# Kernel tuning notes

Measured on AMD Instinct MI355X. Metric: run time of the kernel, lower is better.

Reference implementation:

```python
import jax, jax.numpy as jnp
import numpy as np

ALPHA = 0.25          # VQLayer commitment weight
KL_WEIGHT = 0.01      # settings.kl_weight (repo global)
ENTROPY_WEIGHT = 0.1  # settings.entropy_weight (repo global)


def _forward(x, W0, b0, W1, b1, Wmu, bmu, Wvar, bvar, protos, eps):
    # MLP encoder: input_dim -> 64 -> output_dim, relu after each layer
    h = jax.nn.relu(x @ W0.T + b0)
    h = jax.nn.relu(h @ W1.T + b1)
    logvar = h @ Wvar.T + bvar
    mu = h @ Wmu.T + bmu
    # reparameterize
    latents = mu + eps * jnp.exp(0.5 * logvar)  # [B, D]

    # squared euclidean distances to prototypes: [B, P]
    dists = (jnp.sum(latents ** 2, axis=1, keepdims=True)
             + jnp.sum(protos ** 2, axis=1)
             - 2.0 * latents @ protos.T)
    idx = jnp.argmin(dists, axis=1)              # [B]
    quantized = protos[idx]                      # == one_hot @ protos

    commitment_loss = jnp.mean((jax.lax.stop_gradient(quantized) - latents) ** 2)
    embedding_loss = jnp.mean((quantized - jax.lax.stop_gradient(latents)) ** 2)
    vq_loss = commitment_loss * ALPHA + embedding_loss

    # categorical entropy of mean soft assignment
    logdist = jax.nn.log_softmax(-dists, axis=1)
    soft_dist = jnp.mean(jnp.exp(logdist), axis=0) + 1e-6
    soft_dist = soft_dist / jnp.sum(soft_dist)
    ent = jnp.sum(-soft_dist * jnp.log(soft_dist))
    vq_loss = vq_loss + ENTROPY_WEIGHT * ent

    # straight-through estimator
    quantized = latents + jax.lax.stop_gradient(quantized - latents)

    divergence = jnp.mean(-0.5 * jnp.sum(1.0 + logvar - mu ** 2 - jnp.exp(logvar), axis=1))
    total_loss = KL_WEIGHT * divergence + vq_loss
    return quantized, total_loss, divergence


def setup_inputs() -> dict:
    key = jax.random.key(0)
    ks = jax.random.split(key, 12)
    B, IN, HID, D, P = 32768, 1024, 64, 512, 2048

    def lin(k, fan_in, fan_out):
        bound = 1.0 / np.sqrt(fan_in)
        k1, k2 = jax.random.split(k)
        W = jax.random.uniform(k1, (fan_out, fan_in), jnp.float32, -bound, bound)
        b = jax.random.uniform(k2, (fan_out,), jnp.float32, -bound, bound)
        return W, b

    W0, b0 = lin(ks[0], IN, HID)
    W1, b1 = lin(ks[1], HID, D)
    Wmu, bmu = lin(ks[2], D, D)
    Wvar, bvar = lin(ks[3], D, D)
    protos = jax.random.uniform(ks[4], (P, D), jnp.float32, -1.0 / P, 1.0 / P)
    x = jax.random.normal(ks[5], (B, IN), jnp.float32)
    eps = jax.random.normal(ks[6], (B, D), jnp.float32)
    return {"x": x, "W0": W0, "b0": b0, "W1": W1, "b1": b1,
            "Wmu": Wmu, "bmu": bmu, "Wvar": Wvar, "bvar": bvar,
            "protos": protos, "eps": eps}


def reference(x, W0, b0, W1, b1, Wmu, bmu, Wvar, bvar, protos, eps):
    return _forward(x, W0, b0, W1, b1, Wmu, bmu, Wvar, bvar, protos, eps)
```

## Files before the change

kernel.cpp:

```cpp
#include <hip/hip_runtime.h>
#include <math.h>

#define B_N 32768
#define IN_DIM 1024
#define HID 64
#define D_DIM 512
#define P_N 2048

typedef __attribute__((ext_vector_type(8))) short s16x8;
typedef __attribute__((ext_vector_type(4))) float f32x4;

__device__ __forceinline__ unsigned short f2bf(float f) {
    unsigned u = __float_as_uint(f);
    return (unsigned short)((u + 0x7fffu + ((u >> 16) & 1u)) >> 16);
}
__device__ __forceinline__ float bf2f(unsigned short v) {
    return __uint_as_float(((unsigned)v) << 16);
}

__device__ __forceinline__ void gl_lds(const void* gsrc, void* ldst) {
    __builtin_amdgcn_global_load_lds(
        (const __attribute__((address_space(1))) unsigned int*)gsrc,
        (__attribute__((address_space(3))) unsigned int*)ldst, 16, 0, 0);
}

__device__ __forceinline__ s16x8 pack8(const float* s) {
    float4 x = *(const float4*)s;
    float4 y = *(const float4*)(s + 4);
    s16x8 o;
    o[0] = (short)f2bf(x.x); o[1] = (short)f2bf(x.y);
    o[2] = (short)f2bf(x.z); o[3] = (short)f2bf(x.w);
    o[4] = (short)f2bf(y.x); o[5] = (short)f2bf(y.y);
    o[6] = (short)f2bf(y.z); o[7] = (short)f2bf(y.w);
    return o;
}

__global__ __launch_bounds__(256) void k_prep(const float* __restrict__ protos,
                                              const float* __restrict__ Wmu,
                                              const float* __restrict__ Wvar,
                                              const float* __restrict__ W0,
                                              const float* __restrict__ W1,
                                              unsigned short* __restrict__ pb16,
                                              float* __restrict__ pnorm,
                                              unsigned short* __restrict__ wmv16,
                                              unsigned short* __restrict__ w0pack,
                                              unsigned short* __restrict__ w1pack) {
    int gid = blockIdx.x * 256 + threadIdx.x;
    if (gid < 131072) {
        int row = gid >> 6, k8 = gid & 63;
        const float* s = protos + (size_t)row * 512 + k8 * 8;
        float4 x = *(const float4*)s;
        float4 y = *(const float4*)(s + 4);
        s16x8 o;
        o[0] = (short)f2bf(x.x); o[1] = (short)f2bf(x.y);
        o[2] = (short)f2bf(x.z); o[3] = (short)f2bf(x.w);
        o[4] = (short)f2bf(y.x); o[5] = (short)f2bf(y.y);
        o[6] = (short)f2bf(y.z); o[7] = (short)f2bf(y.w);
        ((s16x8*)pb16)[(size_t)row * 64 + k8] = o;
        float ss = x.x * x.x + x.y * x.y + x.z * x.z + x.w * x.w +
                   y.x * y.x + y.y * y.y + y.z * y.z + y.w * y.w;
#pragma unroll
        for (int d = 1; d < 64; d <<= 1) ss += __shfl_xor(ss, d);
        if ((threadIdx.x & 63) == 0) pnorm[row] = ss;
    } else if (gid < 196608) {
        int a = gid - 131072;
        int row = a >> 6, k8 = a & 63;
        int g = row >> 5, i = row & 31;
        const float* s = (i < 16 ? Wmu + (size_t)(g * 16 + i) * 512
                                 : Wvar + (size_t)(g * 16 + i - 16) * 512) + k8 * 8;
        ((s16x8*)wmv16)[(size_t)row * 64 + k8] = pack8(s);
    } else if (gid < 204800) {
        int a = gid - 196608;
        int row = a >> 7, k8 = a & 127;
        int K32 = k8 >> 2;
        int lane = (row & 15) | ((k8 & 3) << 4);
        ((s16x8*)w0pack)[((size_t)(row >> 4) * 32 + K32) * 64 + lane] =
            pack8(W0 + (size_t)row * IN_DIM + k8 * 8);
    } else {
        int a = gid - 204800;
        int row = a >> 3, k8 = a & 7;
        int K32 = k8 >> 2;
        int lane = (row & 15) | ((k8 & 3) << 4);
        ((s16x8*)w1pack)[((size_t)(row >> 4) * 2 + K32) * 64 + lane] =
            pack8(W1 + (size_t)row * HID + k8 * 8);
    }
}

__global__ __launch_bounds__(256, 4) void k_enc1(const float* __restrict__ x,
                                                 const unsigned short* __restrict__ w0p,
                                                 const float* __restrict__ b0,
                                                 unsigned short* __restrict__ h1b) {
    __shared__ s16x8 As[2048];
    const int tid = threadIdx.x;
    const int l = tid & 63, wid = tid >> 6;
    const int bm = blockIdx.x * 128;
    const s16x8* w0p8 = (const s16x8*)w0p;

    const int srow = tid >> 1, ssub = tid & 1;
    const int srb = srow * 256, ssw = (srow & 7) << 4;

    const int klane = (l >> 4) << 4;
    const int sw = (l & 7) << 4;
    int aoff[2];
#pragma unroll
    for (int m = 0; m < 2; ++m) aoff[m] = (wid * 32 + m * 16 + (l & 15)) * 256;

    f32x4 acc[2][4];
#pragma unroll
    for (int m = 0; m < 2; ++m)
#pragma unroll
        for (int pf = 0; pf < 4; ++pf) acc[m][pf] = (f32x4)0.f;

    for (int kt = 0; kt < 8; ++kt) {
        const float* src = x + (size_t)(bm + srow) * IN_DIM + kt * 128 + ssub * 64;
#pragma unroll
        for (int it = 0; it < 8; ++it) {
            s16x8 o = pack8(src + it * 8);
            int kbyte = ssub * 128 + it * 16;
            As[(srb + (kbyte ^ ssw)) >> 4] = o;
        }
        __syncthreads();
#pragma unroll
        for (int K32 = 0; K32 < 4; ++K32) {
            const int Kg = kt * 4 + K32;
            s16x8 b[4];
#pragma unroll
            for (int pf = 0; pf < 4; ++pf) b[pf] = w0p8[((size_t)pf * 32 + Kg) * 64 + l];
            const int kb = (K32 * 64 + klane) ^ sw;
            s16x8 a[2];
#pragma unroll
            for (int m = 0; m < 2; ++m) a[m] = As[(aoff[m] + kb) >> 4];
#pragma unroll
            for (int m = 0; m < 2; ++m)
#pragma unroll
                for (int pf = 0; pf < 4; ++pf)
                    acc[m][pf] = __builtin_amdgcn_mfma_f32_16x16x32_bf16(a[m], b[pf], acc[m][pf], 0, 0, 0);
        }
        __syncthreads();
    }
#pragma unroll
    for (int m = 0; m < 2; ++m)
#pragma unroll
        for (int pf = 0; pf < 4; ++pf) {
            const int c = pf * 16 + (l & 15);
            const float bb = b0[c];
#pragma unroll
            for (int j = 0; j < 4; ++j) {
                const int r = bm + wid * 32 + m * 16 + (l >> 4) * 4 + j;
                h1b[(size_t)r * HID + c] = f2bf(fmaxf(acc[m][pf][j] + bb, 0.f));
            }
        }
}

__global__ __launch_bounds__(256, 4) void k_enc2(const unsigned short* __restrict__ h1b,
                                                 const unsigned short* __restrict__ w1p,
                                                 const float* __restrict__ b1,
                                                 unsigned short* __restrict__ h2b) {
    __shared__ s16x8 As[512];
    const int tid = threadIdx.x;
    const int l = tid & 63, wid = tid >> 6;
    const int bm = blockIdx.x * 64;
    const s16x8* w1p8 = (const s16x8*)w1p;

#pragma unroll
    for (int it = 0; it < 2; ++it) {
        int g = tid * 2 + it;
        int row = g >> 3, k8 = g & 7;
        s16x8 v = ((const s16x8*)(h1b + (size_t)(bm + row) * HID))[k8];
        As[(row * 128 + ((k8 * 16) ^ ((row & 7) << 4))) >> 4] = v;
    }
    __syncthreads();

    const int arow = wid * 16 + (l & 15);
    const int sw = (l & 7) << 4;
    const int klane = (l >> 4) << 4;
    s16x8 a[2];
#pragma unroll
    for (int K32 = 0; K32 < 2; ++K32)
        a[K32] = As[(arow * 128 + ((K32 * 64 + klane) ^ sw)) >> 4];

    const int r0 = bm + wid * 16 + (l >> 4) * 4;
#pragma unroll
    for (int ct = 0; ct < 4; ++ct) {
        f32x4 acc[8];
#pragma unroll
        for (int pf = 0; pf < 8; ++pf) acc[pf] = (f32x4)0.f;
#pragma unroll
        for (int K32 = 0; K32 < 2; ++K32)
#pragma unroll
            for (int pf = 0; pf < 8; ++pf) {
                s16x8 b = w1p8[(((size_t)(ct * 8 + pf)) * 2 + K32) * 64 + l];
                acc[pf] = __builtin_amdgcn_mfma_f32_16x16x32_bf16(a[K32], b, acc[pf], 0, 0, 0);
            }
#pragma unroll
        for (int pf = 0; pf < 8; ++pf) {
            const int c = ct * 128 + pf * 16 + (l & 15);
            const float bb = b1[c];
#pragma unroll
            for (int j = 0; j < 4; ++j)
                h2b[(size_t)(r0 + j) * D_DIM + c] = f2bf(fmaxf(acc[pf][j] + bb, 0.f));
        }
    }
}

#define GEMM_CORE(Aptr, Bptr)                                                  \
    __shared__ s16x8 A8[1024];                                                 \
    __shared__ s16x8 B8[1024];                                                 \
    const int tid = threadIdx.x;                                               \
    const int l = tid & 63, w = tid >> 6;                                      \
    const int bm = blockIdx.x * 128;                                           \
    const int bn = blockIdx.y * 128;                                           \
    const int wr = w >> 1, wc = w & 1;                                         \
    const int srow = l >> 3;                                                   \
    const int scol = (((l & 7) ^ ((l >> 3) & 7)) * 8);                         \
    f32x4 acc[4][4];                                                           \
    _Pragma("unroll") for (int m = 0; m < 4; ++m)                              \
        _Pragma("unroll") for (int n = 0; n < 4; ++n) acc[m][n] = (f32x4)0.f;  \
    for (int kt = 0; kt < 8; ++kt) {                                           \
        __syncthreads();                                                       \
        _Pragma("unroll") for (int i = 0; i < 4; ++i) {                        \
            const int rb = w * 32 + i * 8;                                     \
            gl_lds(Aptr + (size_t)(bm + rb + srow) * 512 + kt * 64 + scol,     \
                   (char*)A8 + rb * 128);                                      \
            gl_lds(Bptr + (size_t)(bn + rb + srow) * 512 + kt * 64 + scol,     \
                   (char*)B8 + rb * 128);                                      \
        }                                                                      \
        __syncthreads();                                                       \
        _Pragma("unroll") for (int K32 = 0; K32 < 2; ++K32) {                  \
            const int kb = (K32 * 64 + (l >> 4) * 16) ^ ((l & 7) << 4);        \
            s16x8 a[4], b[4];                                                  \
            _Pragma("unroll") for (int m = 0; m < 4; ++m)                      \
                a[m] = A8[((wr * 64 + m * 16 + (l & 15)) * 128 + kb) >> 4];    \
            _Pragma("unroll") for (int n = 0; n < 4; ++n)                      \
                b[n] = B8[((wc * 64 + n * 16 + (l & 15)) * 128 + kb) >> 4];    \
            _Pragma("unroll") for (int m = 0; m < 4; ++m)                      \
                _Pragma("unroll") for (int n = 0; n < 4; ++n)                  \
                    acc[m][n] = __builtin_amdgcn_mfma_f32_16x16x32_bf16(       \
                        a[m], b[n], acc[m][n], 0, 0, 0);                       \
        }                                                                      \
    }

__global__ __launch_bounds__(256, 4) void k_mv(const unsigned short* __restrict__ h2b,
                                               const unsigned short* __restrict__ wmv16,
                                               const float* __restrict__ bmu,
                                               const float* __restrict__ bvar,
                                               const float* __restrict__ eps,
                                               unsigned short* __restrict__ lat16,
                                               float* __restrict__ div_acc) {
    GEMM_CORE(h2b, wmv16)
    __shared__ float red[4];
    float kl = 0.f;
    const int dbase0 = (bn >> 1) + wc * 32;
#pragma unroll
    for (int m = 0; m < 4; ++m)
#pragma unroll
        for (int nn = 0; nn < 2; ++nn) {
            const int d = dbase0 + nn * 16 + (l & 15);
            const float bmv = bmu[d], bvv = bvar[d];
#pragma unroll
            for (int j = 0; j < 4; ++j) {
                const int r = bm + wr * 64 + m * 16 + (l >> 4) * 4 + j;
                float mu = acc[m][2 * nn][j] + bmv;
                float lv = acc[m][2 * nn + 1][j] + bvv;
                float la = fmaf(eps[(size_t)r * D_DIM + d], __expf(0.5f * lv), mu);
                lat16[(size_t)r * D_DIM + d] = f2bf(la);
                kl += mu * mu + __expf(lv) - lv - 1.f;
            }
        }
    kl *= 0.5f;
#pragma unroll
    for (int d = 1; d < 64; d <<= 1) kl += __shfl_xor(kl, d);
    if (l == 0) red[w] = kl;
    __syncthreads();
    if (tid == 0) atomicAdd(div_acc, red[0] + red[1] + red[2] + red[3]);
}

__global__ __launch_bounds__(256, 4) void k_vq1(const unsigned short* __restrict__ lat16,
                                                const unsigned short* __restrict__ pb16,
                                                const float* __restrict__ pnorm,
                                                float* __restrict__ rowS,
                                                unsigned* __restrict__ rowKey,
                                                unsigned short* __restrict__ gA,
                                                unsigned short* __restrict__ gB) {
    GEMM_CORE(lat16, pb16)
    __shared__ float rowS_l[128];
    __shared__ unsigned rowKey_l[128];
    if (tid < 128) { rowS_l[tid] = 0.f; rowKey_l[tid] = 0u; }
    __syncthreads();
    float pn[4];
#pragma unroll
    for (int n = 0; n < 4; ++n) pn[n] = pnorm[bn + wc * 64 + n * 16 + (l & 15)];
    s16x8* gd8 = (s16x8*)((blockIdx.y < 8) ? gA : gB);
    const size_t gbase = ((size_t)((blockIdx.y & 7) * 256 + blockIdx.x) * 8) * 256;
#pragma unroll
    for (int m = 0; m < 4; ++m) {
        float gv[4][4], ev[4][4];
#pragma unroll
        for (int n = 0; n < 4; ++n)
#pragma unroll
            for (int j = 0; j < 4; ++j) {
                gv[n][j] = 2.f * acc[m][n][j] - pn[n];
                ev[n][j] = __expf(gv[n][j]);
            }
        s16x8 u0, u1;
#pragma unroll
        for (int j = 0; j < 4; ++j) {
            u0[j] = (short)f2bf(ev[0][j]); u0[4 + j] = (short)f2bf(ev[1][j]);
            u1[j] = (short)f2bf(ev[2][j]); u1[4 + j] = (short)f2bf(ev[3][j]);
        }
        gd8[gbase + (size_t)(m * 2 + 0) * 256 + tid] = u0;
        gd8[gbase + (size_t)(m * 2 + 1) * 256 + tid] = u1;
#pragma unroll
        for (int j = 0; j < 4; ++j) {
            float se = ev[0][j] + ev[1][j] + ev[2][j] + ev[3][j];
            unsigned key = 0u;
#pragma unroll
            for (int n = 0; n < 4; ++n) {
                const int p = bn + wc * 64 + n * 16 + (l & 15);
                unsigned kk = (__float_as_uint(gv[n][j] + 16.0f) & 0xFFFFF800u) | (unsigned)(2047 - p);
                key = key > kk ? key : kk;
            }
#pragma unroll
            for (int d = 1; d < 16; d <<= 1) {
                se += __shfl_xor(se, d);
                unsigned ok = (unsigned)__shfl_xor((int)key, d);
                key = key > ok ? key : ok;
            }
            if ((l & 15) == 0) {
                const int rloc = wr * 64 + m * 16 + (l >> 4) * 4 + j;
                atomicAdd(&rowS_l[rloc], se);
                atomicMax(&rowKey_l[rloc], key);
            }
        }
    }
    __syncthreads();
    if (tid < 128) {
        atomicAdd(&rowS[bm + tid], rowS_l[tid]);
        atomicMax(&rowKey[bm + tid], rowKey_l[tid]);
    }
}

__global__ __launch_bounds__(256, 4) void k_vq2s(const unsigned short* __restrict__ gA,
                                                 const unsigned short* __restrict__ gB,
                                                 const float* __restrict__ rowS,
                                                 float* __restrict__ soft_acc) {
    __shared__ float soft_l[128];
    const int tid = threadIdx.x;
    const int l = tid & 63, w = tid >> 6;
    const int wr = w >> 1, wc = w & 1;
    const int bm = blockIdx.x * 128;
    const int bn = blockIdx.y * 128;
    if (tid < 128) soft_l[tid] = 0.f;
    __syncthreads();

    const s16x8* gs8 = (const s16x8*)((blockIdx.y < 8) ? gA : gB);
    const size_t gbase = ((size_t)((blockIdx.y & 7) * 256 + blockIdx.x) * 8) * 256;

    float is[4][4];
#pragma unroll
    for (int m = 0; m < 4; ++m)
#pragma unroll
        for (int j = 0; j < 4; ++j)
            is[m][j] = 1.0f / rowS[bm + wr * 64 + m * 16 + (l >> 4) * 4 + j];

    float cs[4] = {0.f, 0.f, 0.f, 0.f};
#pragma unroll
    for (int m = 0; m < 4; ++m) {
        s16x8 u0 = gs8[gbase + (size_t)(m * 2 + 0) * 256 + tid];
        s16x8 u1 = gs8[gbase + (size_t)(m * 2 + 1) * 256 + tid];
#pragma unroll
        for (int j = 0; j < 4; ++j) {
            cs[0] += bf2f((unsigned short)u0[j]) * is[m][j];
            cs[1] += bf2f((unsigned short)u0[4 + j]) * is[m][j];
            cs[2] += bf2f((unsigned short)u1[j]) * is[m][j];
            cs[3] += bf2f((unsigned short)u1[4 + j]) * is[m][j];
        }
    }
#pragma unroll
    for (int n = 0; n < 4; ++n) {
        cs[n] += __shfl_xor(cs[n], 16);
        cs[n] += __shfl_xor(cs[n], 32);
    }
    if (l < 16) {
#pragma unroll
        for (int n = 0; n < 4; ++n) atomicAdd(&soft_l[wc * 64 + n * 16 + l], cs[n]);
    }
    __syncthreads();
    if (tid < 128) atomicAdd(&soft_acc[bn + tid], soft_l[tid]);
}

__global__ __launch_bounds__(256) void k_quant(const float* __restrict__ protos,
                                               const unsigned* __restrict__ rowKey,
                                               const unsigned short* __restrict__ lat16,
                                               float* __restrict__ out,
                                               float* __restrict__ vq_part) {
    const int tid = threadIdx.x;
    const int l = tid & 63, wid = tid >> 6;
    const int base = blockIdx.x * 64;
    float s = 0.f;
#pragma unroll
    for (int it = 0; it < 16; ++it) {
        const int r = base + it * 4 + wid;
        const int p = 2047 - (int)(rowKey[r] & 2047u);
        const float4* qp = (const float4*)(protos + (size_t)p * D_DIM);
        float4* op = (float4*)(out + (size_t)r * D_DIM);
        s16x8 lv = ((const s16x8*)(lat16 + (size_t)r * D_DIM))[l];
        float4 q1 = qp[l * 2], q2 = qp[l * 2 + 1];
        float d0 = q1.x - bf2f((unsigned short)lv[0]);
        float d1 = q1.y - bf2f((unsigned short)lv[1]);
        float d2 = q1.z - bf2f((unsigned short)lv[2]);
        float d3 = q1.w - bf2f((unsigned short)lv[3]);
        float d4 = q2.x - bf2f((unsigned short)lv[4]);
        float d5 = q2.y - bf2f((unsigned short)lv[5]);
        float d6 = q2.z - bf2f((unsigned short)lv[6]);
        float d7 = q2.w - bf2f((unsigned short)lv[7]);
        s += d0 * d0 + d1 * d1 + d2 * d2 + d3 * d3 +
             d4 * d4 + d5 * d5 + d6 * d6 + d7 * d7;
        op[l * 2] = q1; op[l * 2 + 1] = q2;
    }
#pragma unroll
    for (int m = 1; m < 64; m <<= 1) s += __shfl_xor(s, m);
    __shared__ float red[4];
    if (l == 0) red[wid] = s;
    __syncthreads();
    if (tid == 0) vq_part[blockIdx.x] = red[0] + red[1] + red[2] + red[3];
}

__global__ __launch_bounds__(256) void k_final(const float* __restrict__ soft_acc,
                                               const float* __restrict__ scal,
                                               const float* __restrict__ vq_part,
                                               float* __restrict__ out) {
    const int tid = threadIdx.x;
    __shared__ float red[256];
    float vals[8];
    float s = 0.f;
#pragma unroll
    for (int i = 0; i < 8; ++i) {
        float v = soft_acc[tid * 8 + i] * (1.0f / B_N) + 1e-6f;
        vals[i] = v;
        s += v;
    }
    red[tid] = s;
    __syncthreads();
    for (int off = 128; off > 0; off >>= 1) {
        if (tid < off) red[tid] += red[tid + off];
        __syncthreads();
    }
    float norm = red[0];
    __syncthreads();
    float e = 0.f;
#pragma unroll
    for (int i = 0; i < 8; ++i) {
        float p = vals[i] / norm;
        e -= p * __logf(p);
    }
    red[tid] = e;
    __syncthreads();
    for (int off = 128; off > 0; off >>= 1) {
        if (tid < off) red[tid] += red[tid + off];
        __syncthreads();
    }
    float ent = red[0];
    __syncthreads();
    red[tid] = vq_part[tid] + vq_part[tid + 256];
    __syncthreads();
    for (int off = 128; off > 0; off >>= 1) {
        if (tid < off) red[tid] += red[tid + off];
        __syncthreads();
    }
    if (tid == 0) {
        float div = scal[0] * (1.0f / B_N);
        float vq = red[0] * (1.0f / ((float)B_N * (float)D_DIM));
        float vq_loss = 1.25f * vq + 0.1f * ent;
        float total = 0.01f * div + vq_loss;
        out[(size_t)B_N * D_DIM] = total;
        out[(size_t)B_N * D_DIM + 1] = div;
    }
}

extern "C" void kernel_launch(void* const* d_in, const int* in_sizes, int n_in,
                              void* d_out, int out_size, void* d_ws, size_t ws_size,
                              hipStream_t stream) {
    const float* x = (const float*)d_in[0];
    const float* W0 = (const float*)d_in[1];
    const float* b0 = (const float*)d_in[2];
    const float* W1 = (const float*)d_in[3];
    const float* b1 = (const float*)d_in[4];
    const float* Wmu = (const float*)d_in[5];
    const float* bmu = (const float*)d_in[6];
    const float* Wvar = (const float*)d_in[7];
    const float* bvar = (const float*)d_in[8];
    const float* protos = (const float*)d_in[9];
    const float* eps = (const float*)d_in[10];
    float* out = (float*)d_out;

    unsigned short* wsp = (unsigned short*)d_ws;
    unsigned short* lat16 = wsp;
    unsigned short* pb16 = lat16 + (size_t)B_N * D_DIM;
    unsigned short* wmv16 = pb16 + (size_t)P_N * D_DIM;
    unsigned short* w0pack = wmv16 + (size_t)2 * D_DIM * D_DIM;
    unsigned short* w1pack = w0pack + (size_t)HID * IN_DIM;
    float* pnorm = (float*)(w1pack + (size_t)D_DIM * HID);
    float* rowS = pnorm + P_N;
    unsigned* rowKey = (unsigned*)(rowS + B_N);
    float* soft = (float*)(rowKey + B_N);
    float* scal = soft + P_N;
    float* vqpart = scal + 2;
    unsigned short* h1b = (unsigned short*)(vqpart + 512);
    unsigned short* h2b = h1b + (size_t)B_N * HID;
    unsigned short* gA = h1b;
    unsigned short* gB = (unsigned short*)d_out;

    hipMemsetAsync(rowS, 0, (size_t)(B_N * 2 + P_N + 2) * 4, stream);

    k_prep<<<816, 256, 0, stream>>>(protos, Wmu, Wvar, W0, W1,
                                    pb16, pnorm, wmv16, w0pack, w1pack);

    k_enc1<<<B_N / 128, 256, 0, stream>>>(x, w0pack, b0, h1b);
    k_enc2<<<B_N / 64, 256, 0, stream>>>(h1b, w1pack, b1, h2b);

    dim3 gmv(B_N / 128, 8);
    k_mv<<<gmv, 256, 0, stream>>>(h2b, wmv16, bmu, bvar, eps, lat16, scal);

    dim3 gvq(B_N / 128, 16);
    k_vq1<<<gvq, 256, 0, stream>>>(lat16, pb16, pnorm, rowS, rowKey, gA, gB);
    k_vq2s<<<gvq, 256, 0, stream>>>(gA, gB, rowS, soft);

    k_quant<<<B_N / 64, 256, 0, stream>>>(protos, rowKey, lat16, out, vqpart);
    k_final<<<1, 256, 0, stream>>>(soft, scal, vqpart, out);
}
```

Baseline: 309.6 us.

## Fuse encoder layers into one kernel and use nontemporal streaming accesses

Merges the two encoder kernels so the first-layer activations stay in shared memory and go straight into the second GEMM. This drops the h1 global write and read and one launch. The tile per block shrinks to 64 rows, which halves reuse of the W0 fragments loaded from global memory. Separately, the eps reads and the soft-assignment intermediates in the VQ kernels now use nontemporal loads and stores, to reduce cache pollution from streamed data.

```diff
diff --git a/kernel.cpp b/kernel.cpp
--- a/kernel.cpp
+++ b/kernel.cpp
@@ -86,37 +86,35 @@
     }
 }
 
-__global__ __launch_bounds__(256, 4) void k_enc1(const float* __restrict__ x,
-                                                 const unsigned short* __restrict__ w0p,
-                                                 const float* __restrict__ b0,
-                                                 unsigned short* __restrict__ h1b) {
-    __shared__ s16x8 As[2048];
+__global__ __launch_bounds__(256, 4) void k_enc(const float* __restrict__ x,
+                                                const unsigned short* __restrict__ w0p,
+                                                const float* __restrict__ b0,
+                                                const unsigned short* __restrict__ w1p,
+                                                const float* __restrict__ b1,
+                                                unsigned short* __restrict__ h2b) {
+    __shared__ s16x8 As[1024];
     const int tid = threadIdx.x;
     const int l = tid & 63, wid = tid >> 6;
-    const int bm = blockIdx.x * 128;
+    const int bm = blockIdx.x * 64;
     const s16x8* w0p8 = (const s16x8*)w0p;
-
-    const int srow = tid >> 1, ssub = tid & 1;
+    const s16x8* w1p8 = (const s16x8*)w1p;
+
+    const int srow = tid >> 2, ssub = tid & 3;
     const int srb = srow * 256, ssw = (srow & 7) << 4;
-
     const int klane = (l >> 4) << 4;
     const int sw = (l & 7) << 4;
-    int aoff[2];
-#pragma unroll
-    for (int m = 0; m < 2; ++m) aoff[m] = (wid * 32 + m * 16 + (l & 15)) * 256;
-
-    f32x4 acc[2][4];
-#pragma unroll
-    for (int m = 0; m < 2; ++m)
-#pragma unroll
-        for (int pf = 0; pf < 4; ++pf) acc[m][pf] = (f32x4)0.f;
+    const int arow = wid * 16 + (l & 15);
+
+    f32x4 acc1[4];
+#pragma unroll
+    for (int pf = 0; pf < 4; ++pf) acc1[pf] = (f32x4)0.f;
 
     for (int kt = 0; kt < 8; ++kt) {
-        const float* src = x + (size_t)(bm + srow) * IN_DIM + kt * 128 + ssub * 64;
-#pragma unroll
-        for (int it = 0; it < 8; ++it) {
+        const float* src = x + (size_t)(bm + srow) * IN_DIM + kt * 128 + ssub * 32;
+#pragma unroll
+        for (int it = 0; it < 4; ++it) {
             s16x8 o = pack8(src + it * 8);
-            int kbyte = ssub * 128 + it * 16;
+            int kbyte = ssub * 64 + it * 16;
             As[(srb + (kbyte ^ ssw)) >> 4] = o;
         }
         __syncthreads();
@@ -126,71 +124,48 @@
             s16x8 b[4];
 #pragma unroll
             for (int pf = 0; pf < 4; ++pf) b[pf] = w0p8[((size_t)pf * 32 + Kg) * 64 + l];
-            const int kb = (K32 * 64 + klane) ^ sw;
-            s16x8 a[2];
-#pragma unroll
-            for (int m = 0; m < 2; ++m) a[m] = As[(aoff[m] + kb) >> 4];
-#pragma unroll
-            for (int m = 0; m < 2; ++m)
-#pragma unroll
-                for (int pf = 0; pf < 4; ++pf)
-                    acc[m][pf] = __builtin_amdgcn_mfma_f32_16x16x32_bf16(a[m], b[pf], acc[m][pf], 0, 0, 0);
+            s16x8 a = As[(arow * 256 + ((K32 * 64 + klane) ^ sw)) >> 4];
+#pragma unroll
+            for (int pf = 0; pf < 4; ++pf)
+                acc1[pf] = __builtin_amdgcn_mfma_f32_16x16x32_bf16(a, b[pf], acc1[pf], 0, 0, 0);
         }
         __syncthreads();
     }
-#pragma unroll
-    for (int m = 0; m < 2; ++m)
+
+    {
+        unsigned short* Hs = (unsigned short*)As;
 #pragma unroll
         for (int pf = 0; pf < 4; ++pf) {
             const int c = pf * 16 + (l & 15);
             const float bb = b0[c];
 #pragma unroll
             for (int j = 0; j < 4; ++j) {
-                const int r = bm + wid * 32 + m * 16 + (l >> 4) * 4 + j;
-                h1b[(size_t)r * HID + c] = f2bf(fmaxf(acc[m][pf][j] + bb, 0.f));
-            }
-        }
-}
-
-__global__ __launch_bounds__(256, 4) void k_enc2(const unsigned short* __restrict__ h1b,
-                                                 const unsigned short* __restrict__ w1p,
-                                                 const float* __restrict__ b1,
-                                                 unsigned short* __restrict__ h2b) {
-    __shared__ s16x8 As[512];
-    const int tid = threadIdx.x;
-    const int l = tid & 63, wid = tid >> 6;
-    const int bm = blockIdx.x * 64;
-    const s16x8* w1p8 = (const s16x8*)w1p;
-
-#pragma unroll
-    for (int it = 0; it < 2; ++it) {
-        int g = tid * 2 + it;
-        int row = g >> 3, k8 = g & 7;
-        s16x8 v = ((const s16x8*)(h1b + (size_t)(bm + row) * HID))[k8];
-        As[(row * 128 + ((k8 * 16) ^ ((row & 7) << 4))) >> 4] = v;
-    }
-    __syncthreads();
-
-    const int arow = wid * 16 + (l & 15);
-    const int sw = (l & 7) << 4;
-    const int klane = (l >> 4) << 4;
-    s16x8 a[2];
+                const int r = wid * 16 + (l >> 4) * 4 + j;
+                float v = fmaxf(acc1[pf][j] + bb, 0.f);
+                int byte = r * 128 + ((c * 2) ^ ((r & 7) << 4));
+                Hs[byte >> 1] = f2bf(v);
+            }
+        }
+    }
+    __syncthreads();
+
+    s16x8 a2[2];
 #pragma unroll
     for (int K32 = 0; K32 < 2; ++K32)
-        a[K32] = As[(arow * 128 + ((K32 * 64 + klane) ^ sw)) >> 4];
+        a2[K32] = As[(arow * 128 + ((K32 * 64 + klane) ^ sw)) >> 4];
 
     const int r0 = bm + wid * 16 + (l >> 4) * 4;
 #pragma unroll
     for (int ct = 0; ct < 4; ++ct) {
-        f32x4 acc[8];
-#pragma unroll
-        for (int pf = 0; pf < 8; ++pf) acc[pf] = (f32x4)0.f;
+        f32x4 acc2[8];
+#pragma unroll
+        for (int pf = 0; pf < 8; ++pf) acc2[pf] = (f32x4)0.f;
 #pragma unroll
         for (int K32 = 0; K32 < 2; ++K32)
 #pragma unroll
             for (int pf = 0; pf < 8; ++pf) {
                 s16x8 b = w1p8[(((size_t)(ct * 8 + pf)) * 2 + K32) * 64 + l];
-                acc[pf] = __builtin_amdgcn_mfma_f32_16x16x32_bf16(a[K32], b, acc[pf], 0, 0, 0);
+                acc2[pf] = __builtin_amdgcn_mfma_f32_16x16x32_bf16(a2[K32], b, acc2[pf], 0, 0, 0);
             }
 #pragma unroll
         for (int pf = 0; pf < 8; ++pf) {
@@ -198,7 +173,7 @@
             const float bb = b1[c];
 #pragma unroll
             for (int j = 0; j < 4; ++j)
-                h2b[(size_t)(r0 + j) * D_DIM + c] = f2bf(fmaxf(acc[pf][j] + bb, 0.f));
+                h2b[(size_t)(r0 + j) * D_DIM + c] = f2bf(fmaxf(acc2[pf][j] + bb, 0.f));
         }
     }
 }
@@ -262,7 +237,8 @@
                 const int r = bm + wr * 64 + m * 16 + (l >> 4) * 4 + j;
                 float mu = acc[m][2 * nn][j] + bmv;
                 float lv = acc[m][2 * nn + 1][j] + bvv;
-                float la = fmaf(eps[(size_t)r * D_DIM + d], __expf(0.5f * lv), mu);
+                float ev = __builtin_nontemporal_load(&eps[(size_t)r * D_DIM + d]);
+                float la = fmaf(ev, __expf(0.5f * lv), mu);
                 lat16[(size_t)r * D_DIM + d] = f2bf(la);
                 kl += mu * mu + __expf(lv) - lv - 1.f;
             }
@@ -308,8 +284,8 @@
             u0[j] = (short)f2bf(ev[0][j]); u0[4 + j] = (short)f2bf(ev[1][j]);
             u1[j] = (short)f2bf(ev[2][j]); u1[4 + j] = (short)f2bf(ev[3][j]);
         }
-        gd8[gbase + (size_t)(m * 2 + 0) * 256 + tid] = u0;
-        gd8[gbase + (size_t)(m * 2 + 1) * 256 + tid] = u1;
+        __builtin_nontemporal_store(u0, &gd8[gbase + (size_t)(m * 2 + 0) * 256 + tid]);
+        __builtin_nontemporal_store(u1, &gd8[gbase + (size_t)(m * 2 + 1) * 256 + tid]);
 #pragma unroll
         for (int j = 0; j < 4; ++j) {
             float se = ev[0][j] + ev[1][j] + ev[2][j] + ev[3][j];
@@ -366,8 +342,8 @@
     float cs[4] = {0.f, 0.f, 0.f, 0.f};
 #pragma unroll
     for (int m = 0; m < 4; ++m) {
-        s16x8 u0 = gs8[gbase + (size_t)(m * 2 + 0) * 256 + tid];
-        s16x8 u1 = gs8[gbase + (size_t)(m * 2 + 1) * 256 + tid];
+        s16x8 u0 = __builtin_nontemporal_load(&gs8[gbase + (size_t)(m * 2 + 0) * 256 + tid]);
+        s16x8 u1 = __builtin_nontemporal_load(&gs8[gbase + (size_t)(m * 2 + 1) * 256 + tid]);
 #pragma unroll
         for (int j = 0; j < 4; ++j) {
             cs[0] += bf2f((unsigned short)u0[j]) * is[m][j];
@@ -506,9 +482,9 @@
     float* soft = (float*)(rowKey + B_N);
     float* scal = soft + P_N;
     float* vqpart = scal + 2;
-    unsigned short* h1b = (unsigned short*)(vqpart + 512);
-    unsigned short* h2b = h1b + (size_t)B_N * HID;
-    unsigned short* gA = h1b;
+    unsigned short* h2b = (unsigned short*)(vqpart + 512) +
+                          (size_t)B_N * HID;
+    unsigned short* gA = (unsigned short*)(vqpart + 512);
     unsigned short* gB = (unsigned short*)d_out;
 
     hipMemsetAsync(rowS, 0, (size_t)(B_N * 2 + P_N + 2) * 4, stream);
@@ -516,8 +492,7 @@
     k_prep<<<816, 256, 0, stream>>>(protos, Wmu, Wvar, W0, W1,
                                     pb16, pnorm, wmv16, w0pack, w1pack);
 
-    k_enc1<<<B_N / 128, 256, 0, stream>>>(x, w0pack, b0, h1b);
-    k_enc2<<<B_N / 64, 256, 0, stream>>>(h1b, w1pack, b1, h2b);
+    k_enc<<<B_N / 64, 256, 0, stream>>>(x, w0pack, b0, w1pack, b1, h2b);
 
     dim3 gmv(B_N / 128, 8);
     k_mv<<<gmv, 256, 0, stream>>>(h2b, wmv16, bmu, bvar, eps, lat16, scal);
```

Measured after the change: 292.7 us (median of 2 runs). 5.4% less time.
